# Performance work log

Measured on AMD Instinct MI355X. Metric: run time of the kernel, lower is better.

## Reference

```python
import jax, jax.numpy as jnp
import numpy as np

B, D, T = 16, 512, 4096
N_CB, K, CDIM = 9, 1024, 8
EPS = 1e-12  # F.normalize eps


def setup_inputs() -> dict:
    key = jax.random.key(0)
    ks = jax.random.split(key, 6)
    z = jax.random.normal(ks[0], (B, D, T), dtype=jnp.float32)
    # Effective (post weight-norm) 1x1-conv weights per codebook, stacked over N_CB
    w_in = jax.random.normal(ks[1], (N_CB, CDIM, D), dtype=jnp.float32) * 0.02
    b_in = jax.random.normal(ks[2], (N_CB, CDIM), dtype=jnp.float32) * 0.02
    w_out = jax.random.normal(ks[3], (N_CB, D, CDIM), dtype=jnp.float32) * 0.02
    b_out = jax.random.normal(ks[4], (N_CB, D), dtype=jnp.float32) * 0.02
    codebooks = jax.random.normal(ks[5], (N_CB, K, CDIM), dtype=jnp.float32)
    return {"z": z, "w_in": w_in, "b_in": b_in, "w_out": w_out,
            "b_out": b_out, "codebooks": codebooks}


def _l2norm(x):
    return x / jnp.maximum(jnp.linalg.norm(x, axis=-1, keepdims=True), EPS)


def reference(z, w_in, b_in, w_out, b_out, codebooks):
    """Eval-mode RVQ forward with all n_codebooks quantizers (mask all-True).
    Returns (z_q, codes, latents, commitment_loss, codebook_loss)."""
    Bz, _, Tz = z.shape

    def step(carry, params):
        residual, zq_acc, cl, cbl = carry
        wi, bi, wo, bo, cb = params
        # in_proj: 1x1 conv input_dim -> codebook_dim
        z_e = jnp.einsum('cd,bdt->bct', wi, residual) + bi[None, :, None]  # B,CDIM,T
        enc = z_e.transpose(0, 2, 1).reshape(-1, z_e.shape[1])            # (B*T),CDIM
        en = _l2norm(enc)
        cbn = _l2norm(cb)
        # squared euclidean distance on l2-normalized vectors (cosine dist)
        dist = ((en * en).sum(1, keepdims=True)
                - 2.0 * (en @ cbn.T)
                + (cbn * cbn).sum(1)[None, :])                            # (B*T),K
        idx = jnp.argmin(dist, axis=1).reshape(Bz, Tz)                    # B,T
        z_q_i = cb[idx].transpose(0, 2, 1)                                # B,CDIM,T (raw codebook)
        cl = cl + jnp.mean((z_e - jax.lax.stop_gradient(z_q_i)) ** 2, axis=(1, 2)).mean()
        cbl = cbl + jnp.mean((z_q_i - jax.lax.stop_gradient(z_e)) ** 2, axis=(1, 2)).mean()
        # straight-through estimator
        z_q_st = z_e + jax.lax.stop_gradient(z_q_i - z_e)
        z_q_out = jnp.einsum('dc,bct->bdt', wo, z_q_st) + bo[None, :, None]  # B,D,T
        return (residual - z_q_out, zq_acc + z_q_out, cl, cbl), (idx, z_e)

    init = (z, jnp.zeros_like(z), jnp.float32(0.0), jnp.float32(0.0))
    (_, z_q, cl, cbl), (codes, latents) = jax.lax.scan(
        step, init, (w_in, b_in, w_out, b_out, codebooks))
    codes = codes.transpose(1, 0, 2)                         # B,N,T
    latents = latents.transpose(1, 0, 2, 3).reshape(Bz, -1, Tz)  # B,N*CDIM,T
    return z_q, codes, latents, cl, cbl
```

## Files before the change

### kernel.cpp

```cpp
#include <hip/hip_runtime.h>
#include <math.h>

#define Bz  16
#define Dz  512
#define Tz  4096
#define NCB 9
#define Kz  1024
#define CD  8

static const unsigned long long OZQ   = 0ull;
static const unsigned long long OCODE = 33554432ull;
static const unsigned long long OLAT  = 34144256ull;
static const unsigned long long OCL   = 38862848ull;

#define WS_CBN2_OFF (NCB * CD * Kz)

__global__ __launch_bounds__(1024) void rvq_prep(const float* __restrict__ cb,
                                                 float* __restrict__ ws,
                                                 float* __restrict__ out) {
    const int i = blockIdx.x;
    const int k = threadIdx.x;
    const float* row = cb + ((size_t)i * Kz + k) * CD;
    float v[CD];
#pragma unroll
    for (int c = 0; c < CD; ++c) v[c] = row[c];
    float ss = 0.f;
#pragma unroll
    for (int c = 0; c < CD; ++c) ss += v[c] * v[c];
    const float den = fmaxf(sqrtf(ss), 1e-12f);
    float cb2 = 0.f;
#pragma unroll
    for (int c = 0; c < CD; ++c) {
        float e = v[c] / den;
        ws[((size_t)i * CD + c) * Kz + k] = e;
        cb2 += e * e;
    }
    ws[WS_CBN2_OFF + (size_t)i * Kz + k] = cb2;
    if (i == 0 && k == 0) { out[OCL] = 0.f; out[OCL + 1] = 0.f; }
}

__global__ __launch_bounds__(1024)
void rvq_main(
    const float* __restrict__ z,
    const float* __restrict__ w_in,
    const float* __restrict__ b_in,
    const float* __restrict__ w_out,
    const float* __restrict__ b_out,
    const float* __restrict__ cb,
    const float* __restrict__ ws,
    float* __restrict__ out)
{
    __shared__ float s_win[64 * 68];
    __shared__ float s_cbnT[8 * 64 * 20];
    __shared__ float s_cbn2[Kz];
    __shared__ float s_lat[8 * 33];
    __shared__ float s_code[NCB * 32];
    __shared__ float s_red[16];

    float* s_tr = s_cbnT;

    const int tid  = threadIdx.x;
    const int wave = tid >> 6;
    const int lane = tid & 63;
    const int bb   = blockIdx.x;
    const int b    = bb >> 7;
    const int t0blk = (bb & 127) << 5;
    const int mycol = lane & 1;

    const size_t zbase = (size_t)b * Dz * Tz + t0blk;

    float res2[2][8];
#pragma unroll 1
    for (int c = 0; c < 4; ++c) {
        {
            const int r = tid >> 3;
            const int u = (tid & 7) * 4;
            float4 v = *(const float4*)(z + zbase + (size_t)(c * 128 + r) * Tz + u);
            s_tr[(u + 0) * 132 + r] = v.x;
            s_tr[(u + 1) * 132 + r] = v.y;
            s_tr[(u + 2) * 132 + r] = v.z;
            s_tr[(u + 3) * 132 + r] = v.w;
        }
        __syncthreads();
        if ((lane >> 4) == c) {
            const int lr = (lane & 15) * 8;
#pragma unroll
            for (int col = 0; col < 2; ++col)
#pragma unroll
                for (int j = 0; j < 8; ++j)
                    res2[col][j] = s_tr[(wave * 2 + col) * 132 + lr + j];
        }
        __syncthreads();
    }

    float lsum = 0.f;

#pragma unroll 1
    for (int i = 0; i < NCB; ++i) {
        __syncthreads();
        if (i > 0 && tid < 256) {
            const int c2 = tid >> 5, u = tid & 31;
            out[OLAT + ((size_t)b * 72 + (i - 1) * 8 + c2) * Tz + t0blk + u] =
                s_lat[c2 * 33 + u];
        }
        {
            const float4* src = (const float4*)(w_in + (size_t)i * 4096);
            {
                int e4 = tid;
                float4 v = src[e4];
                int e = e4 * 4, c = e >> 9, d = e & 511;
                *(float4*)&s_win[(d >> 3) * 68 + c * 8 + (d & 7)] = v;
            }
            const float4* srcT = (const float4*)(ws + (size_t)i * 8192);
#pragma unroll
            for (int it = 0; it < 2; ++it) {
                int e4 = tid + it * 1024;
                float4 v = srcT[e4];
                int e = e4 * 4, c = e >> 10, k = e & 1023;
                *(float4*)&s_cbnT[c * 1280 + (k >> 4) * 20 + (k & 15)] = v;
            }
            if (tid < 256) {
                const float4* s2 = (const float4*)(ws + WS_CBN2_OFF + (size_t)i * Kz);
                ((float4*)s_cbn2)[tid] = s2[tid];
            }
        }
        __syncthreads();

        float z_own[8];
#pragma unroll
        for (int c = 0; c < 8; ++c) {
            const float* wl = &s_win[lane * 68 + c * 8];
            float4 a = *(const float4*)wl;
            float4 b4 = *(const float4*)(wl + 4);
            float w8[8] = {a.x, a.y, a.z, a.w, b4.x, b4.y, b4.z, b4.w};
            float q[2];
#pragma unroll
            for (int col = 0; col < 2; ++col) {
                float s = 0.f;
#pragma unroll
                for (int j = 0; j < 8; ++j) s = fmaf(w8[j], res2[col][j], s);
                q[col] = s;
            }
            q[0] += __shfl_xor(q[0], 1, 64);
            q[1] += __shfl_xor(q[1], 1, 64);
            float v = mycol ? q[1] : q[0];
#pragma unroll
            for (int off = 2; off <= 32; off <<= 1) v += __shfl_xor(v, off, 64);
            z_own[c] = v + b_in[i * 8 + c];
        }

        {
            int cc = lane >> 1;
            float v = z_own[0];
#pragma unroll
            for (int c = 1; c < 8; ++c) v = (cc == c) ? z_own[c] : v;
            if (lane < 16) s_lat[cc * 33 + wave * 2 + mycol] = v;
        }

        float ss = 0.f;
#pragma unroll
        for (int c = 0; c < 8; ++c) ss += z_own[c] * z_own[c];
        const float den = fmaxf(sqrtf(ss), 1e-12f);
        float en_own[8];
#pragma unroll
        for (int c = 0; c < 8; ++c) en_own[c] = z_own[c] / den;

        float en2[2][8];
        const int qb = lane & ~1;
#pragma unroll
        for (int g = 0; g < 2; ++g) {
#pragma unroll
            for (int c = 0; c < 8; ++c) en2[g][c] = __shfl(en_own[c], qb + g, 64);
        }

        float best[2]; int bidx[2];
#pragma unroll
        for (int g = 0; g < 2; ++g) { best[g] = 1e30f; bidx[g] = 0; }
#pragma unroll
        for (int mq = 0; mq < 4; ++mq) {
            float4 c2 = *(const float4*)&s_cbn2[lane * 16 + mq * 4];
            float dots[2][4];
#pragma unroll
            for (int g = 0; g < 2; ++g)
#pragma unroll
                for (int q = 0; q < 4; ++q) dots[g][q] = 0.f;
#pragma unroll
            for (int c = 0; c < 8; ++c) {
                float4 v = *(const float4*)&s_cbnT[c * 1280 + lane * 20 + mq * 4];
#pragma unroll
                for (int g = 0; g < 2; ++g) {
                    dots[g][0] = fmaf(en2[g][c], v.x, dots[g][0]);
                    dots[g][1] = fmaf(en2[g][c], v.y, dots[g][1]);
                    dots[g][2] = fmaf(en2[g][c], v.z, dots[g][2]);
                    dots[g][3] = fmaf(en2[g][c], v.w, dots[g][3]);
                }
            }
#pragma unroll
            for (int q = 0; q < 4; ++q) {
                const int kk = lane * 16 + mq * 4 + q;
                const float cb2q = (q == 0) ? c2.x : (q == 1) ? c2.y : (q == 2) ? c2.z : c2.w;
#pragma unroll
                for (int g = 0; g < 2; ++g) {
                    float dist = fmaf(-2.f, dots[g][q], cb2q);
                    if (dist < best[g]) { best[g] = dist; bidx[g] = kk; }
                }
            }
        }
#pragma unroll
        for (int off = 1; off <= 32; off <<= 1) {
#pragma unroll
            for (int g = 0; g < 2; ++g) {
                float ob = __shfl_xor(best[g], off, 64);
                int   oi = __shfl_xor(bidx[g], off, 64);
                if (ob < best[g] || (ob == best[g] && oi < bidx[g])) {
                    best[g] = ob; bidx[g] = oi;
                }
            }
        }

        float cbq[2][8];
#pragma unroll
        for (int g = 0; g < 2; ++g) {
            const float* cr = cb + ((size_t)i * Kz + bidx[g]) * CD;
            float4 a = *(const float4*)cr;
            float4 b4 = *(const float4*)(cr + 4);
            cbq[g][0] = a.x;  cbq[g][1] = a.y;  cbq[g][2] = a.z;  cbq[g][3] = a.w;
            cbq[g][4] = b4.x; cbq[g][5] = b4.y; cbq[g][6] = b4.z; cbq[g][7] = b4.w;
        }

#pragma unroll
        for (int g = 0; g < 2; ++g) {
            if (lane == g) {
#pragma unroll
                for (int c = 0; c < 8; ++c) {
                    float dd = z_own[c] - cbq[g][c];
                    lsum = fmaf(dd, dd, lsum);
                }
            }
        }

        {
            float v = (float)bidx[0];
            v = (lane == 1) ? (float)bidx[1] : v;
            if (lane < 2) s_code[i * 32 + wave * 2 + lane] = v;
        }

        {
            const float* wo = w_out + (size_t)i * 4096 + (size_t)lane * 64;
            const float* bo = b_out + (size_t)i * Dz + lane * 8;
            float4 bA = *(const float4*)bo;
            float4 bB = *(const float4*)(bo + 4);
            float bv[8] = {bA.x, bA.y, bA.z, bA.w, bB.x, bB.y, bB.z, bB.w};
#pragma unroll
            for (int j = 0; j < 8; ++j) {
                float4 wa = *(const float4*)(wo + j * 8);
                float4 wb = *(const float4*)(wo + j * 8 + 4);
                float wr[8] = {wa.x, wa.y, wa.z, wa.w, wb.x, wb.y, wb.z, wb.w};
#pragma unroll
                for (int g = 0; g < 2; ++g) {
                    float s = 0.f;
#pragma unroll
                    for (int c = 0; c < 8; ++c) s = fmaf(wr[c], cbq[g][c], s);
                    res2[g][j] -= (s + bv[j]);
                }
            }
        }
    }

    __syncthreads();
    if (tid < 256) {
        const int c2 = tid >> 5, u = tid & 31;
        out[OLAT + ((size_t)b * 72 + 8 * 8 + c2) * Tz + t0blk + u] = s_lat[c2 * 33 + u];
    }
    if (tid < NCB * 32) {
        const int i2 = tid >> 5, u = tid & 31;
        out[OCODE + ((size_t)b * NCB + i2) * Tz + t0blk + u] = s_code[i2 * 32 + u];
    }

#pragma unroll 1
    for (int c = 0; c < 4; ++c) {
        if ((lane >> 4) == c) {
            const int lr = (lane & 15) * 8;
#pragma unroll
            for (int col = 0; col < 2; ++col)
#pragma unroll
                for (int j = 0; j < 8; ++j)
                    s_tr[(wave * 2 + col) * 132 + lr + j] = res2[col][j];
        }
        __syncthreads();
        {
            const int r = tid >> 3;
            const int u = (tid & 7) * 4;
            float4 zv = *(const float4*)(z + zbase + (size_t)(c * 128 + r) * Tz + u);
            float4 v;
            v.x = zv.x - s_tr[(u + 0) * 132 + r];
            v.y = zv.y - s_tr[(u + 1) * 132 + r];
            v.z = zv.z - s_tr[(u + 2) * 132 + r];
            v.w = zv.w - s_tr[(u + 3) * 132 + r];
            *(float4*)(out + OZQ + zbase + (size_t)(c * 128 + r) * Tz + u) = v;
        }
        __syncthreads();
    }

#pragma unroll
    for (int off = 1; off <= 32; off <<= 1) lsum += __shfl_xor(lsum, off, 64);
    if (lane == 0) s_red[wave] = lsum;
    __syncthreads();
    if (tid == 0) {
        float t = 0.f;
#pragma unroll
        for (int w2 = 0; w2 < 16; ++w2) t += s_red[w2];
        t *= (1.f / 524288.f);
        atomicAdd(&out[OCL], t);
        atomicAdd(&out[OCL + 1], t);
    }
}

extern "C" void kernel_launch(void* const* d_in, const int* in_sizes, int n_in,
                              void* d_out, int out_size, void* d_ws, size_t ws_size,
                              hipStream_t stream) {
    (void)in_sizes; (void)n_in; (void)out_size; (void)ws_size;
    const float* z     = (const float*)d_in[0];
    const float* w_in  = (const float*)d_in[1];
    const float* b_in  = (const float*)d_in[2];
    const float* w_out = (const float*)d_in[3];
    const float* b_out = (const float*)d_in[4];
    const float* cb    = (const float*)d_in[5];
    float* ws  = (float*)d_ws;
    float* out = (float*)d_out;

    rvq_prep<<<NCB, 1024, 0, stream>>>(cb, ws, out);
    rvq_main<<<2048, 1024, 0, stream>>>(z, w_in, b_in, w_out, b_out, cb, ws, out);
}
```

Baseline: 1.370 ms.

## Use DPP wave reductions and register-direct latent/code writes in RVQ kernel

Replaces the shfl_xor butterfly reductions with DPP row/bcast reductions plus readlane, for the in_proj sums, the argmin and the loss. The argmin is now a wave min followed by a ballot on the lowest lane. w_in and the codebook norms are read straight from global memory instead of being staged in LDS, and latents and codes are written directly rather than through LDS buffers. The aim is fewer cross-lane shuffles, less LDS traffic and less staging per codebook step, at the cost of scattered 4-byte global stores and more global loads.

```diff
diff --git a/kernel.cpp b/kernel.cpp
--- a/kernel.cpp
+++ b/kernel.cpp
@@ -37,6 +37,36 @@
     }
     ws[WS_CBN2_OFF + (size_t)i * Kz + k] = cb2;
     if (i == 0 && k == 0) { out[OCL] = 0.f; out[OCL + 1] = 0.f; }
+}
+
+template <int CTRL>
+__device__ __forceinline__ float dpp_add_t(float v) {
+    int t = __builtin_amdgcn_update_dpp(0, __float_as_int(v), CTRL, 0xf, 0xf, true);
+    return v + __int_as_float(t);
+}
+__device__ __forceinline__ float wave_sum64(float v) {
+    v = dpp_add_t<0x111>(v);
+    v = dpp_add_t<0x112>(v);
+    v = dpp_add_t<0x114>(v);
+    v = dpp_add_t<0x118>(v);
+    v = dpp_add_t<0x142>(v);
+    v = dpp_add_t<0x143>(v);
+    return __int_as_float(__builtin_amdgcn_readlane(__float_as_int(v), 63));
+}
+template <int CTRL>
+__device__ __forceinline__ float dpp_min_t(float v) {
+    int t = __builtin_amdgcn_update_dpp(__float_as_int(v), __float_as_int(v),
+                                        CTRL, 0xf, 0xf, false);
+    return fminf(v, __int_as_float(t));
+}
+__device__ __forceinline__ float wave_min64(float v) {
+    v = dpp_min_t<0x111>(v);
+    v = dpp_min_t<0x112>(v);
+    v = dpp_min_t<0x114>(v);
+    v = dpp_min_t<0x118>(v);
+    v = dpp_min_t<0x142>(v);
+    v = dpp_min_t<0x143>(v);
+    return __int_as_float(__builtin_amdgcn_readlane(__float_as_int(v), 63));
 }
 
 __global__ __launch_bounds__(1024)
@@ -50,13 +80,8 @@
     const float* __restrict__ ws,
     float* __restrict__ out)
 {
-    __shared__ float s_win[64 * 68];
-    __shared__ float s_cbnT[8 * 64 * 20];
-    __shared__ float s_cbn2[Kz];
-    __shared__ float s_lat[8 * 33];
-    __shared__ float s_code[NCB * 32];
+    __shared__ float s_cbnT[CD * Kz];
     __shared__ float s_red[16];
-
     float* s_tr = s_cbnT;
 
     const int tid  = threadIdx.x;
@@ -65,7 +90,6 @@
     const int bb   = blockIdx.x;
     const int b    = bb >> 7;
     const int t0blk = (bb & 127) << 5;
-    const int mycol = lane & 1;
 
     const size_t zbase = (size_t)b * Dz * Tz + t0blk;
 
@@ -98,151 +122,142 @@
 #pragma unroll 1
     for (int i = 0; i < NCB; ++i) {
         __syncthreads();
-        if (i > 0 && tid < 256) {
-            const int c2 = tid >> 5, u = tid & 31;
-            out[OLAT + ((size_t)b * 72 + (i - 1) * 8 + c2) * Tz + t0blk + u] =
-                s_lat[c2 * 33 + u];
-        }
-        {
-            const float4* src = (const float4*)(w_in + (size_t)i * 4096);
-            {
-                int e4 = tid;
-                float4 v = src[e4];
-                int e = e4 * 4, c = e >> 9, d = e & 511;
-                *(float4*)&s_win[(d >> 3) * 68 + c * 8 + (d & 7)] = v;
-            }
+        {
             const float4* srcT = (const float4*)(ws + (size_t)i * 8192);
-#pragma unroll
-            for (int it = 0; it < 2; ++it) {
-                int e4 = tid + it * 1024;
-                float4 v = srcT[e4];
-                int e = e4 * 4, c = e >> 10, k = e & 1023;
-                *(float4*)&s_cbnT[c * 1280 + (k >> 4) * 20 + (k & 15)] = v;
-            }
-            if (tid < 256) {
-                const float4* s2 = (const float4*)(ws + WS_CBN2_OFF + (size_t)i * Kz);
-                ((float4*)s_cbn2)[tid] = s2[tid];
-            }
-        }
-        __syncthreads();
-
-        float z_own[8];
+            float4 v0 = srcT[tid];
+            float4 v1 = srcT[tid + 1024];
+            ((float4*)s_cbnT)[tid]        = v0;
+            ((float4*)s_cbnT)[tid + 1024] = v1;
+        }
+        __syncthreads();
+
+        float zz[2][8];
+        {
+            const float* wb = w_in + (size_t)i * 4096 + lane * 8;
+#pragma unroll
+            for (int c = 0; c < 8; ++c) {
+                float4 wa = *(const float4*)(wb + c * 512);
+                float4 wc = *(const float4*)(wb + c * 512 + 4);
+                float q0 = wa.x * res2[0][0];
+                float q1 = wa.x * res2[1][0];
+                q0 = fmaf(wa.y, res2[0][1], q0); q1 = fmaf(wa.y, res2[1][1], q1);
+                q0 = fmaf(wa.z, res2[0][2], q0); q1 = fmaf(wa.z, res2[1][2], q1);
+                q0 = fmaf(wa.w, res2[0][3], q0); q1 = fmaf(wa.w, res2[1][3], q1);
+                q0 = fmaf(wc.x, res2[0][4], q0); q1 = fmaf(wc.x, res2[1][4], q1);
+                q0 = fmaf(wc.y, res2[0][5], q0); q1 = fmaf(wc.y, res2[1][5], q1);
+                q0 = fmaf(wc.z, res2[0][6], q0); q1 = fmaf(wc.z, res2[1][6], q1);
+                q0 = fmaf(wc.w, res2[0][7], q0); q1 = fmaf(wc.w, res2[1][7], q1);
+                zz[0][c] = wave_sum64(q0);
+                zz[1][c] = wave_sum64(q1);
+            }
+            float4 bA = *(const float4*)(b_in + i * 8);
+            float4 bB = *(const float4*)(b_in + i * 8 + 4);
+            zz[0][0] += bA.x; zz[1][0] += bA.x;
+            zz[0][1] += bA.y; zz[1][1] += bA.y;
+            zz[0][2] += bA.z; zz[1][2] += bA.z;
+            zz[0][3] += bA.w; zz[1][3] += bA.w;
+            zz[0][4] += bB.x; zz[1][4] += bB.x;
+            zz[0][5] += bB.y; zz[1][5] += bB.y;
+            zz[0][6] += bB.z; zz[1][6] += bB.z;
+            zz[0][7] += bB.w; zz[1][7] += bB.w;
+        }
+
+        {
+            float v = zz[0][0];
+            v = (lane == 1)  ? zz[1][0] : v;
+            v = (lane == 2)  ? zz[0][1] : v;
+            v = (lane == 3)  ? zz[1][1] : v;
+            v = (lane == 4)  ? zz[0][2] : v;
+            v = (lane == 5)  ? zz[1][2] : v;
+            v = (lane == 6)  ? zz[0][3] : v;
+            v = (lane == 7)  ? zz[1][3] : v;
+            v = (lane == 8)  ? zz[0][4] : v;
+            v = (lane == 9)  ? zz[1][4] : v;
+            v = (lane == 10) ? zz[0][5] : v;
+            v = (lane == 11) ? zz[1][5] : v;
+            v = (lane == 12) ? zz[0][6] : v;
+            v = (lane == 13) ? zz[1][6] : v;
+            v = (lane == 14) ? zz[0][7] : v;
+            v = (lane == 15) ? zz[1][7] : v;
+            if (lane < 16)
+                out[OLAT + ((size_t)b * 72 + i * 8 + (lane >> 1)) * Tz
+                    + t0blk + wave * 2 + (lane & 1)] = v;
+        }
+
+        float ss0 = 0.f, ss1 = 0.f;
 #pragma unroll
         for (int c = 0; c < 8; ++c) {
-            const float* wl = &s_win[lane * 68 + c * 8];
-            float4 a = *(const float4*)wl;
-            float4 b4 = *(const float4*)(wl + 4);
-            float w8[8] = {a.x, a.y, a.z, a.w, b4.x, b4.y, b4.z, b4.w};
-            float q[2];
-#pragma unroll
-            for (int col = 0; col < 2; ++col) {
-                float s = 0.f;
-#pragma unroll
-                for (int j = 0; j < 8; ++j) s = fmaf(w8[j], res2[col][j], s);
-                q[col] = s;
-            }
-            q[0] += __shfl_xor(q[0], 1, 64);
-            q[1] += __shfl_xor(q[1], 1, 64);
-            float v = mycol ? q[1] : q[0];
-#pragma unroll
-            for (int off = 2; off <= 32; off <<= 1) v += __shfl_xor(v, off, 64);
-            z_own[c] = v + b_in[i * 8 + c];
-        }
-
-        {
-            int cc = lane >> 1;
-            float v = z_own[0];
-#pragma unroll
-            for (int c = 1; c < 8; ++c) v = (cc == c) ? z_own[c] : v;
-            if (lane < 16) s_lat[cc * 33 + wave * 2 + mycol] = v;
-        }
-
-        float ss = 0.f;
-#pragma unroll
-        for (int c = 0; c < 8; ++c) ss += z_own[c] * z_own[c];
-        const float den = fmaxf(sqrtf(ss), 1e-12f);
-        float en_own[8];
-#pragma unroll
-        for (int c = 0; c < 8; ++c) en_own[c] = z_own[c] / den;
-
-        float en2[2][8];
-        const int qb = lane & ~1;
-#pragma unroll
-        for (int g = 0; g < 2; ++g) {
-#pragma unroll
-            for (int c = 0; c < 8; ++c) en2[g][c] = __shfl(en_own[c], qb + g, 64);
-        }
-
-        float best[2]; int bidx[2];
-#pragma unroll
-        for (int g = 0; g < 2; ++g) { best[g] = 1e30f; bidx[g] = 0; }
+            ss0 = fmaf(zz[0][c], zz[0][c], ss0);
+            ss1 = fmaf(zz[1][c], zz[1][c], ss1);
+        }
+        const float den0 = fmaxf(sqrtf(ss0), 1e-12f);
+        const float den1 = fmaxf(sqrtf(ss1), 1e-12f);
+        float en[2][8];
+#pragma unroll
+        for (int c = 0; c < 8; ++c) {
+            en[0][c] = zz[0][c] / den0;
+            en[1][c] = zz[1][c] / den1;
+        }
+
+        float best0 = 1e30f, best1 = 1e30f;
+        int   bi0 = 0, bi1 = 0;
+        const float* c2base = ws + WS_CBN2_OFF + (size_t)i * Kz;
 #pragma unroll
         for (int mq = 0; mq < 4; ++mq) {
-            float4 c2 = *(const float4*)&s_cbn2[lane * 16 + mq * 4];
-            float dots[2][4];
-#pragma unroll
-            for (int g = 0; g < 2; ++g)
-#pragma unroll
-                for (int q = 0; q < 4; ++q) dots[g][q] = 0.f;
+            const int kb = mq * 256 + lane * 4;
+            float4 c2 = *(const float4*)(c2base + kb);
+            float d00 = 0.f, d01 = 0.f, d02 = 0.f, d03 = 0.f;
+            float d10 = 0.f, d11 = 0.f, d12 = 0.f, d13 = 0.f;
 #pragma unroll
             for (int c = 0; c < 8; ++c) {
-                float4 v = *(const float4*)&s_cbnT[c * 1280 + lane * 20 + mq * 4];
-#pragma unroll
-                for (int g = 0; g < 2; ++g) {
-                    dots[g][0] = fmaf(en2[g][c], v.x, dots[g][0]);
-                    dots[g][1] = fmaf(en2[g][c], v.y, dots[g][1]);
-                    dots[g][2] = fmaf(en2[g][c], v.z, dots[g][2]);
-                    dots[g][3] = fmaf(en2[g][c], v.w, dots[g][3]);
-                }
-            }
-#pragma unroll
-            for (int q = 0; q < 4; ++q) {
-                const int kk = lane * 16 + mq * 4 + q;
-                const float cb2q = (q == 0) ? c2.x : (q == 1) ? c2.y : (q == 2) ? c2.z : c2.w;
-#pragma unroll
-                for (int g = 0; g < 2; ++g) {
-                    float dist = fmaf(-2.f, dots[g][q], cb2q);
-                    if (dist < best[g]) { best[g] = dist; bidx[g] = kk; }
-                }
-            }
-        }
-#pragma unroll
-        for (int off = 1; off <= 32; off <<= 1) {
-#pragma unroll
-            for (int g = 0; g < 2; ++g) {
-                float ob = __shfl_xor(best[g], off, 64);
-                int   oi = __shfl_xor(bidx[g], off, 64);
-                if (ob < best[g] || (ob == best[g] && oi < bidx[g])) {
-                    best[g] = ob; bidx[g] = oi;
-                }
-            }
-        }
-
-        float cbq[2][8];
-#pragma unroll
-        for (int g = 0; g < 2; ++g) {
-            const float* cr = cb + ((size_t)i * Kz + bidx[g]) * CD;
-            float4 a = *(const float4*)cr;
-            float4 b4 = *(const float4*)(cr + 4);
-            cbq[g][0] = a.x;  cbq[g][1] = a.y;  cbq[g][2] = a.z;  cbq[g][3] = a.w;
-            cbq[g][4] = b4.x; cbq[g][5] = b4.y; cbq[g][6] = b4.z; cbq[g][7] = b4.w;
-        }
-
-#pragma unroll
-        for (int g = 0; g < 2; ++g) {
-            if (lane == g) {
-#pragma unroll
-                for (int c = 0; c < 8; ++c) {
-                    float dd = z_own[c] - cbq[g][c];
-                    lsum = fmaf(dd, dd, lsum);
-                }
-            }
-        }
-
-        {
-            float v = (float)bidx[0];
-            v = (lane == 1) ? (float)bidx[1] : v;
-            if (lane < 2) s_code[i * 32 + wave * 2 + lane] = v;
+                float4 v = *(const float4*)&s_cbnT[c * 1024 + kb];
+                d00 = fmaf(en[0][c], v.x, d00); d10 = fmaf(en[1][c], v.x, d10);
+                d01 = fmaf(en[0][c], v.y, d01); d11 = fmaf(en[1][c], v.y, d11);
+                d02 = fmaf(en[0][c], v.z, d02); d12 = fmaf(en[1][c], v.z, d12);
+                d03 = fmaf(en[0][c], v.w, d03); d13 = fmaf(en[1][c], v.w, d13);
+            }
+            float dist;
+            dist = fmaf(-2.f, d00, c2.x); if (dist < best0) { best0 = dist; bi0 = kb + 0; }
+            dist = fmaf(-2.f, d01, c2.y); if (dist < best0) { best0 = dist; bi0 = kb + 1; }
+            dist = fmaf(-2.f, d02, c2.z); if (dist < best0) { best0 = dist; bi0 = kb + 2; }
+            dist = fmaf(-2.f, d03, c2.w); if (dist < best0) { best0 = dist; bi0 = kb + 3; }
+            dist = fmaf(-2.f, d10, c2.x); if (dist < best1) { best1 = dist; bi1 = kb + 0; }
+            dist = fmaf(-2.f, d11, c2.y); if (dist < best1) { best1 = dist; bi1 = kb + 1; }
+            dist = fmaf(-2.f, d12, c2.z); if (dist < best1) { best1 = dist; bi1 = kb + 2; }
+            dist = fmaf(-2.f, d13, c2.w); if (dist < best1) { best1 = dist; bi1 = kb + 3; }
+        }
+        const float g0 = wave_min64(best0);
+        const float g1 = wave_min64(best1);
+        const int wl0 = __ffsll((long long)(unsigned long long)__ballot(best0 == g0)) - 1;
+        const int wl1 = __ffsll((long long)(unsigned long long)__ballot(best1 == g1)) - 1;
+        const int k0 = __builtin_amdgcn_readlane(bi0, wl0);
+        const int k1 = __builtin_amdgcn_readlane(bi1, wl1);
+
+        const float* cr0 = cb + ((size_t)i * Kz + k0) * CD;
+        float4 qa = *(const float4*)cr0, qb = *(const float4*)(cr0 + 4);
+        float cq0[8] = {qa.x, qa.y, qa.z, qa.w, qb.x, qb.y, qb.z, qb.w};
+        const float* cr1 = cb + ((size_t)i * Kz + k1) * CD;
+        float4 qc = *(const float4*)cr1, qd = *(const float4*)(cr1 + 4);
+        float cq1[8] = {qc.x, qc.y, qc.z, qc.w, qd.x, qd.y, qd.z, qd.w};
+
+        if (lane == 0) {
+            out[OCODE + ((size_t)b * NCB + i) * Tz + t0blk + wave * 2]     = (float)k0;
+            out[OCODE + ((size_t)b * NCB + i) * Tz + t0blk + wave * 2 + 1] = (float)k1;
+        }
+
+        if (lane == 0) {
+#pragma unroll
+            for (int c = 0; c < 8; ++c) {
+                float dd = en[0][c] * den0 - cq0[c];
+                lsum = fmaf(dd, dd, lsum);
+            }
+        }
+        if (lane == 1) {
+#pragma unroll
+            for (int c = 0; c < 8; ++c) {
+                float dd = en[1][c] * den1 - cq1[c];
+                lsum = fmaf(dd, dd, lsum);
+            }
         }
 
         {
@@ -253,30 +268,24 @@
             float bv[8] = {bA.x, bA.y, bA.z, bA.w, bB.x, bB.y, bB.z, bB.w};
 #pragma unroll
             for (int j = 0; j < 8; ++j) {
-                float4 wa = *(const float4*)(wo + j * 8);
-                float4 wb = *(const float4*)(wo + j * 8 + 4);
-                float wr[8] = {wa.x, wa.y, wa.z, wa.w, wb.x, wb.y, wb.z, wb.w};
-#pragma unroll
-                for (int g = 0; g < 2; ++g) {
-                    float s = 0.f;
-#pragma unroll
-                    for (int c = 0; c < 8; ++c) s = fmaf(wr[c], cbq[g][c], s);
-                    res2[g][j] -= (s + bv[j]);
-                }
+                float4 wa  = *(const float4*)(wo + j * 8);
+                float4 wb2 = *(const float4*)(wo + j * 8 + 4);
+                float s0 = wa.x * cq0[0];
+                float s1 = wa.x * cq1[0];
+                s0 = fmaf(wa.y,  cq0[1], s0); s1 = fmaf(wa.y,  cq1[1], s1);
+                s0 = fmaf(wa.z,  cq0[2], s0); s1 = fmaf(wa.z,  cq1[2], s1);
+                s0 = fmaf(wa.w,  cq0[3], s0); s1 = fmaf(wa.w,  cq1[3], s1);
+                s0 = fmaf(wb2.x, cq0[4], s0); s1 = fmaf(wb2.x, cq1[4], s1);
+                s0 = fmaf(wb2.y, cq0[5], s0); s1 = fmaf(wb2.y, cq1[5], s1);
+                s0 = fmaf(wb2.z, cq0[6], s0); s1 = fmaf(wb2.z, cq1[6], s1);
+                s0 = fmaf(wb2.w, cq0[7], s0); s1 = fmaf(wb2.w, cq1[7], s1);
+                res2[0][j] -= (s0 + bv[j]);
+                res2[1][j] -= (s1 + bv[j]);
             }
         }
     }
 
     __syncthreads();
-    if (tid < 256) {
-        const int c2 = tid >> 5, u = tid & 31;
-        out[OLAT + ((size_t)b * 72 + 8 * 8 + c2) * Tz + t0blk + u] = s_lat[c2 * 33 + u];
-    }
-    if (tid < NCB * 32) {
-        const int i2 = tid >> 5, u = tid & 31;
-        out[OCODE + ((size_t)b * NCB + i2) * Tz + t0blk + u] = s_code[i2 * 32 + u];
-    }
-
 #pragma unroll 1
     for (int c = 0; c < 4; ++c) {
         if ((lane >> 4) == c) {
@@ -302,9 +311,8 @@
         __syncthreads();
     }
 
-#pragma unroll
-    for (int off = 1; off <= 32; off <<= 1) lsum += __shfl_xor(lsum, off, 64);
-    if (lane == 0) s_red[wave] = lsum;
+    float lt = wave_sum64(lsum);
+    if (lane == 0) s_red[wave] = lt;
     __syncthreads();
     if (tid == 0) {
         float t = 0.f;
```

Measured after the change: 1.508 ms. +10.0%, slower.
